# Optimization experiments

Measured on AMD Instinct MI355X. Metric: run time of the kernel, lower is better.

The kernel has to match this reference:

```python
import jax, jax.numpy as jnp
import numpy as np
import math

B, S, D = 16, 1, 4096
H, KVH, HD = 32, 8, 128
MAXB, MAXS = 16, 4096
R = H // KVH  # n_rep


def _rope(t, cos, sin):
    # t: [B, S, h, HD]; cos/sin: [S, HD//2]
    tf = t.astype(jnp.float32).reshape(*t.shape[:-1], HD // 2, 2)
    a, b = tf[..., 0], tf[..., 1]
    c = cos[None, :, None, :]
    s = sin[None, :, None, :]
    out = jnp.stack([a * c - b * s, a * s + b * c], axis=-1)
    return out.reshape(t.shape).astype(t.dtype)


def setup_inputs() -> dict:
    key = jax.random.key(0)
    ks = jax.random.split(key, 9)
    scale = 1.0 / math.sqrt(D)
    ang = jax.random.uniform(ks[7], (S, HD // 2), jnp.float32) * (2.0 * np.pi)
    return {
        "x": jax.random.normal(ks[0], (B, S, D), jnp.float32),
        "start_pos": 4095,
        "freqs_cos": jnp.cos(ang),
        "freqs_sin": jnp.sin(ang),
        "cache_k": jax.random.normal(ks[1], (MAXB, MAXS, KVH, HD), jnp.float32),
        "cache_v": jax.random.normal(ks[2], (MAXB, MAXS, KVH, HD), jnp.float32),
        "wq": jax.random.normal(ks[3], (D, H * HD), jnp.float32) * scale,
        "wk": jax.random.normal(ks[4], (D, KVH * HD), jnp.float32) * scale,
        "wv": jax.random.normal(ks[5], (D, KVH * HD), jnp.float32) * scale,
        "wo": jax.random.normal(ks[6], (H * HD, D), jnp.float32) * scale,
    }


def reference(x, start_pos, freqs_cos, freqs_sin, cache_k, cache_v, wq, wk, wv, wo):
    bsz, seqlen, _ = x.shape
    xq = (x @ wq).reshape(bsz, seqlen, H, HD)
    xk = (x @ wk).reshape(bsz, seqlen, KVH, HD)
    xv = (x @ wv).reshape(bsz, seqlen, KVH, HD)
    # rotary embeddings on q and k
    xq = _rope(xq, freqs_cos, freqs_sin)
    xk = _rope(xk, freqs_cos, freqs_sin)
    # KV-cache write (start_pos is a static Python int)
    cache_k = cache_k.at[:bsz, start_pos:start_pos + seqlen].set(xk)
    cache_v = cache_v.at[:bsz, start_pos:start_pos + seqlen].set(xv)
    T = start_pos + seqlen
    keys = cache_k[:bsz, :T]    # [B, T, KVH, HD]
    values = cache_v[:bsz, :T]  # [B, T, KVH, HD]
    # GQA: group q heads as [KVH, R] instead of materializing repeated K/V
    q = xq.reshape(bsz, seqlen, KVH, R, HD)
    scores = jnp.einsum("bsgrd,btgd->bgrst", q, keys) / math.sqrt(HD)
    probs = jax.nn.softmax(scores.astype(jnp.float32), axis=-1).astype(xq.dtype)
    out = jnp.einsum("bgrst,btgd->bsgrd", probs, values)
    out = out.reshape(bsz, seqlen, H * HD)
    return out @ wo
```

## Files before the change

kernel.cpp:

```cpp
#include <hip/hip_runtime.h>
#include <hip/hip_bf16.h>
#include <math.h>

#define B 16
#define D 4096
#define H 32
#define KVH 8
#define HD 128
#define R 4
#define T 4096
#define NQKV 6144
#define NCH_A 32
#define NCH_E 32
#define NCH64 64
#define MREC 516

#define OFF_QKV   0
#define SZ_QKV    (B*NQKV)
#define OFF_ATTN  (OFF_QKV + SZ_QKV)
#define SZ_ATTN   (B*H*HD)
#define OFF_MLO   (OFF_ATTN + SZ_ATTN)
#define SZ_MLO    (B*KVH*NCH64*MREC)
#define OFF_PART  (OFF_ATTN + SZ_ATTN)

__global__ __launch_bounds__(256) void gemv_qkv(
    const float* __restrict__ x, const float* __restrict__ wq,
    const float* __restrict__ wk, const float* __restrict__ wv,
    float* __restrict__ part) {
  int cb = blockIdx.x;
  int ch = blockIdx.y;
  int d0 = ch * 128;
  __shared__ float xT[128][20];
  for (int i = threadIdx.x; i < 128*B; i += 256) {
    int b = i >> 7;
    int d = i & 127;
    xT[d][b] = x[b*D + d0 + d];
  }
  __syncthreads();
  const float* W; int ncols, colbase, outbase;
  if (cb < 16)      { W = wq; ncols = 4096; colbase = cb*256;      outbase = colbase; }
  else if (cb < 20) { W = wk; ncols = 1024; colbase = (cb-16)*256; outbase = 4096 + colbase; }
  else              { W = wv; ncols = 1024; colbase = (cb-20)*256; outbase = 5120 + colbase; }
  int j = colbase + threadIdx.x;
  const float* wp = W + (size_t)d0*ncols + j;
  float acc[16];
  #pragma unroll
  for (int b = 0; b < 16; ++b) acc[b] = 0.f;
  for (int dd = 0; dd < 128; dd += 8) {
    float w[8];
    #pragma unroll
    for (int u = 0; u < 8; ++u) w[u] = wp[(size_t)u*ncols];
    wp += (size_t)8*ncols;
    #pragma unroll
    for (int u = 0; u < 8; ++u) {
      int d = dd + u;
      #pragma unroll
      for (int bq = 0; bq < 4; ++bq) {
        float4 xb = *(const float4*)&xT[d][bq*4];
        acc[bq*4+0] += w[u]*xb.x;
        acc[bq*4+1] += w[u]*xb.y;
        acc[bq*4+2] += w[u]*xb.z;
        acc[bq*4+3] += w[u]*xb.w;
      }
    }
  }
  int outcol = outbase + threadIdx.x;
  #pragma unroll
  for (int b = 0; b < 16; ++b) {
    part[(size_t)ch*SZ_QKV + b*NQKV + outcol] = acc[b];
  }
}

__global__ __launch_bounds__(256) void reduce_rope(
    const float* __restrict__ part, float* __restrict__ qkv,
    const float* __restrict__ fc, const float* __restrict__ fs) {
  int i = blockIdx.x*256 + threadIdx.x;
  int flat = i*2;
  float2 s = make_float2(0.f, 0.f);
  for (int c = 0; c < NCH_A; ++c) {
    float2 v = *(const float2*)&part[(size_t)c*SZ_QKV + flat];
    s.x += v.x; s.y += v.y;
  }
  int col = flat % NQKV;
  if (col < 5120) {
    int jj = (col & 127) >> 1;
    float c = fc[jj], sn = fs[jj];
    float ox = s.x*c - s.y*sn;
    float oy = s.x*sn + s.y*c;
    if (col < 4096) { ox *= 0.08838834764831845f; oy *= 0.08838834764831845f; }
    s.x = ox; s.y = oy;
  }
  *(float2*)&qkv[flat] = s;
}

__global__ __launch_bounds__(256) void attn_kernel(
    const float* __restrict__ qkv, const float* __restrict__ cache_k,
    const float* __restrict__ cache_v, float* __restrict__ mlo) {
  int chunk = blockIdx.x, gh = blockIdx.y, b = blockIdx.z;
  int tid = threadIdx.x, wave = tid >> 6, lane = tid & 63;
  int g = gh*4 + wave;
  int t0 = chunk * 64;
  __shared__ float4 q_lds4[4][4][32];
  __shared__ float4 p_lds[4][64];

  {
    const float* qp = qkv + b*NQKV + g*R*HD;
    int f = lane*2;
    q_lds4[wave][f>>5][f&31] = *(const float4*)(qp + f*4);
    f++;
    q_lds4[wave][f>>5][f&31] = *(const float4*)(qp + f*4);
  }

  const float* knew = qkv + b*NQKV + 4096 + g*HD;
  const float* vnew = qkv + b*NQKV + 5120 + g*HD;
  size_t base = ((size_t)(b*KVH + g)*NCH64 + chunk)*MREC;

  {
    int sub = lane & 7, rloc = lane >> 3;
    float l4[4] = {0.f,0.f,0.f,0.f};
    #pragma unroll 2
    for (int p = 0; p < 8; ++p) {
      int row = p*8 + rloc;
      int t = t0 + row;
      const float* kp = (t == T-1) ? knew
                        : &cache_k[(((size_t)b*T + t)*KVH + g)*HD];
      float4 kreg[4];
      #pragma unroll
      for (int i = 0; i < 4; ++i) kreg[i] = ((const float4*)kp)[i*8 + sub];
      float sA[4] = {0.f,0.f,0.f,0.f};
      #pragma unroll
      for (int i = 0; i < 4; ++i) {
        #pragma unroll
        for (int h = 0; h < 4; ++h) {
          float4 qv = q_lds4[wave][h][i*8 + sub];
          sA[h] += kreg[i].x*qv.x + kreg[i].y*qv.y + kreg[i].z*qv.z + kreg[i].w*qv.w;
        }
      }
      #pragma unroll
      for (int h = 0; h < 4; ++h) {
        sA[h] += __shfl_xor(sA[h], 1);
        sA[h] += __shfl_xor(sA[h], 2);
        sA[h] += __shfl_xor(sA[h], 4);
        sA[h] = __expf(sA[h]);
        l4[h] += sA[h];
      }
      if (sub == 0) p_lds[wave][row] = make_float4(sA[0], sA[1], sA[2], sA[3]);
    }
    #pragma unroll
    for (int h = 0; h < 4; ++h) {
      l4[h] += __shfl_xor(l4[h], 8);
      l4[h] += __shfl_xor(l4[h], 16);
      l4[h] += __shfl_xor(l4[h], 32);
    }
    if (lane == 0) {
      mlo[base + 0] = l4[0]; mlo[base + 1] = l4[1];
      mlo[base + 2] = l4[2]; mlo[base + 3] = l4[3];
    }
  }

  {
    int sub = lane & 31, rhalf = lane >> 5;
    float4 acc4[4];
    #pragma unroll
    for (int h = 0; h < 4; ++h) acc4[h] = make_float4(0.f,0.f,0.f,0.f);
    #pragma unroll 2
    for (int bt = 0; bt < 8; ++bt) {
      float4 vreg[4];
      #pragma unroll
      for (int i = 0; i < 4; ++i) {
        int row = bt*8 + i*2 + rhalf;
        int t = t0 + row;
        const float* vrow = (t == T-1) ? vnew
                           : &cache_v[(((size_t)b*T + t)*KVH + g)*HD];
        vreg[i] = *(const float4*)&vrow[sub*4];
      }
      #pragma unroll
      for (int i = 0; i < 4; ++i) {
        int row = bt*8 + i*2 + rhalf;
        float4 p = p_lds[wave][row];
        acc4[0].x += p.x*vreg[i].x; acc4[0].y += p.x*vreg[i].y;
        acc4[0].z += p.x*vreg[i].z; acc4[0].w += p.x*vreg[i].w;
        acc4[1].x += p.y*vreg[i].x; acc4[1].y += p.y*vreg[i].y;
        acc4[1].z += p.y*vreg[i].z; acc4[1].w += p.y*vreg[i].w;
        acc4[2].x += p.z*vreg[i].x; acc4[2].y += p.z*vreg[i].y;
        acc4[2].z += p.z*vreg[i].z; acc4[2].w += p.z*vreg[i].w;
        acc4[3].x += p.w*vreg[i].x; acc4[3].y += p.w*vreg[i].y;
        acc4[3].z += p.w*vreg[i].z; acc4[3].w += p.w*vreg[i].w;
      }
    }
    #pragma unroll
    for (int h = 0; h < 4; ++h) {
      acc4[h].x += __shfl_xor(acc4[h].x, 32);
      acc4[h].y += __shfl_xor(acc4[h].y, 32);
      acc4[h].z += __shfl_xor(acc4[h].z, 32);
      acc4[h].w += __shfl_xor(acc4[h].w, 32);
    }
    if (rhalf == 0) {
      #pragma unroll
      for (int h = 0; h < 4; ++h)
        *(float4*)&mlo[base + 4 + h*HD + sub*4] = acc4[h];
    }
  }
}

__global__ __launch_bounds__(128) void combine_kernel(
    const float* __restrict__ mlo, float* __restrict__ attn) {
  int g = blockIdx.x, b = blockIdx.y;
  int d = threadIdx.x;
  size_t b0 = (size_t)(b*KVH + g)*NCH64*MREC;
  #pragma unroll
  for (int h = 0; h < 4; ++h) {
    float l = 0.f, o = 0.f;
    for (int c = 0; c < NCH64; ++c) {
      size_t bb = b0 + (size_t)c*MREC;
      l += mlo[bb + h];
      o += mlo[bb + 4 + h*HD + d];
    }
    attn[b*D + (g*R + h)*HD + d] = o / l;
  }
}

__global__ __launch_bounds__(256) void gemv_out(
    const float* __restrict__ attn, const float* __restrict__ wo,
    float* __restrict__ part) {
  int cb = blockIdx.x;
  int ch = blockIdx.y;
  int d0 = ch * 128;
  __shared__ float xT[128][20];
  for (int i = threadIdx.x; i < 128*B; i += 256) {
    int b = i >> 7;
    int d = i & 127;
    xT[d][b] = attn[b*D + d0 + d];
  }
  __syncthreads();
  int j = cb*256 + threadIdx.x;
  const float* wp = wo + (size_t)d0*D + j;
  float acc[16];
  #pragma unroll
  for (int b = 0; b < 16; ++b) acc[b] = 0.f;
  for (int dd = 0; dd < 128; dd += 8) {
    float w[8];
    #pragma unroll
    for (int u = 0; u < 8; ++u) w[u] = wp[(size_t)u*D];
    wp += (size_t)8*D;
    #pragma unroll
    for (int u = 0; u < 8; ++u) {
      int d = dd + u;
      #pragma unroll
      for (int bq = 0; bq < 4; ++bq) {
        float4 xb = *(const float4*)&xT[d][bq*4];
        acc[bq*4+0] += w[u]*xb.x;
        acc[bq*4+1] += w[u]*xb.y;
        acc[bq*4+2] += w[u]*xb.z;
        acc[bq*4+3] += w[u]*xb.w;
      }
    }
  }
  #pragma unroll
  for (int b = 0; b < 16; ++b) {
    part[(size_t)ch*SZ_ATTN + b*D + j] = acc[b];
  }
}

__global__ __launch_bounds__(256) void reduce_part(
    const float* __restrict__ part, float* __restrict__ out, int n, int nch) {
  int i = (blockIdx.x*256 + threadIdx.x)*4;
  if (i >= n) return;
  float4 s = make_float4(0.f,0.f,0.f,0.f);
  for (int c = 0; c < nch; ++c) {
    float4 v = *(const float4*)&part[(size_t)c*n + i];
    s.x += v.x; s.y += v.y; s.z += v.z; s.w += v.w;
  }
  *(float4*)&out[i] = s;
}

extern "C" void kernel_launch(void* const* d_in, const int* in_sizes, int n_in,
                              void* d_out, int out_size, void* d_ws, size_t ws_size,
                              hipStream_t stream) {
  const float* x  = (const float*)d_in[0];
  const float* fc = (const float*)d_in[2];
  const float* fs = (const float*)d_in[3];
  const float* ck = (const float*)d_in[4];
  const float* cv = (const float*)d_in[5];
  const float* wq = (const float*)d_in[6];
  const float* wk = (const float*)d_in[7];
  const float* wv = (const float*)d_in[8];
  const float* wo = (const float*)d_in[9];
  float* out  = (float*)d_out;
  float* ws   = (float*)d_ws;
  float* qkv  = ws + OFF_QKV;
  float* attn = ws + OFF_ATTN;
  float* mlo  = ws + OFF_MLO;
  float* part = ws + OFF_PART;

  gemv_qkv<<<dim3(24, NCH_A), 256, 0, stream>>>(x, wq, wk, wv, part);
  reduce_rope<<<dim3(SZ_QKV/512), 256, 0, stream>>>(part, qkv, fc, fs);
  attn_kernel<<<dim3(NCH64, 2, B), 256, 0, stream>>>(qkv, ck, cv, mlo);
  combine_kernel<<<dim3(KVH, B), 128, 0, stream>>>(mlo, attn);
  gemv_out<<<dim3(16, NCH_E), 256, 0, stream>>>(attn, wo, part);
  reduce_part<<<dim3(SZ_ATTN/1024), 256, 0, stream>>>(part, out, SZ_ATTN, NCH_E);
}
```

Baseline: 183.8 us.

## Restructure decode attention: one block per batch chunk over all KV heads, with max-stabilized softmax

Each attention block now covers all 8 KV heads for a 64-token chunk of one batch, so every K/V row (1024 contiguous floats) is read fully coalesced. K is staged through LDS with a one-step register prefetch. Scores go to a shared score tile, and a per-chunk max-subtracted softmax replaces the unstabilized exp. The combine kernel now rescales each chunk by its max and runs one block per query head. The trade-offs are fewer, larger blocks (1024 instead of 2048), more LDS per block, extra syncthreads, and a larger partial-result record per chunk.

```diff
diff --git a/kernel.cpp b/kernel.cpp
--- a/kernel.cpp
+++ b/kernel.cpp
@@ -13,14 +13,14 @@
 #define NCH_A 32
 #define NCH_E 32
 #define NCH64 64
-#define MREC 516
+#define MREC 4160
 
 #define OFF_QKV   0
 #define SZ_QKV    (B*NQKV)
 #define OFF_ATTN  (OFF_QKV + SZ_QKV)
 #define SZ_ATTN   (B*H*HD)
 #define OFF_MLO   (OFF_ATTN + SZ_ATTN)
-#define SZ_MLO    (B*KVH*NCH64*MREC)
+#define SZ_MLO    (B*NCH64*MREC)
 #define OFF_PART  (OFF_ATTN + SZ_ATTN)
 
 __global__ __launch_bounds__(256) void gemv_qkv(
@@ -96,44 +96,56 @@
 __global__ __launch_bounds__(256) void attn_kernel(
     const float* __restrict__ qkv, const float* __restrict__ cache_k,
     const float* __restrict__ cache_v, float* __restrict__ mlo) {
-  int chunk = blockIdx.x, gh = blockIdx.y, b = blockIdx.z;
+  int chunk = blockIdx.x, b = blockIdx.y;
   int tid = threadIdx.x, wave = tid >> 6, lane = tid & 63;
-  int g = gh*4 + wave;
   int t0 = chunk * 64;
-  __shared__ float4 q_lds4[4][4][32];
-  __shared__ float4 p_lds[4][64];
+  int g0 = wave * 2;
+  __shared__ float4 ktile[4][4][2][35];
+  __shared__ float score[64][36];
+
+  size_t base = ((size_t)b*NCH64 + chunk)*MREC;
 
   {
-    const float* qp = qkv + b*NQKV + g*R*HD;
-    int f = lane*2;
-    q_lds4[wave][f>>5][f&31] = *(const float4*)(qp + f*4);
-    f++;
-    q_lds4[wave][f>>5][f&31] = *(const float4*)(qp + f*4);
-  }
-
-  const float* knew = qkv + b*NQKV + 4096 + g*HD;
-  const float* vnew = qkv + b*NQKV + 5120 + g*HD;
-  size_t base = ((size_t)(b*KVH + g)*NCH64 + chunk)*MREC;
-
-  {
-    int sub = lane & 7, rloc = lane >> 3;
-    float l4[4] = {0.f,0.f,0.f,0.f};
-    #pragma unroll 2
-    for (int p = 0; p < 8; ++p) {
-      int row = p*8 + rloc;
-      int t = t0 + row;
-      const float* kp = (t == T-1) ? knew
-                        : &cache_k[(((size_t)b*T + t)*KVH + g)*HD];
-      float4 kreg[4];
-      #pragma unroll
-      for (int i = 0; i < 4; ++i) kreg[i] = ((const float4*)kp)[i*8 + sub];
+    int sub = lane & 7, rowg = lane >> 3;
+    int krow = rowg >> 1, kgsel = rowg & 1;
+    int kg = g0 + kgsel;
+    float4 qreg[4][4];
+    #pragma unroll
+    for (int h = 0; h < 4; ++h)
+      #pragma unroll
+      for (int i = 0; i < 4; ++i)
+        qreg[h][i] = *(const float4*)(qkv + b*NQKV + (kg*4 + h)*HD + (i*8 + sub)*4);
+
+    const float* kbase = cache_k + (size_t)b*T*1024 + g0*HD;
+    const float* knew  = qkv + b*NQKV + 4096 + g0*HD;
+    float4 cur[4];
+    #pragma unroll
+    for (int ii = 0; ii < 4; ++ii) {
+      int t = t0 + ii;
+      const float* src = (t == T-1) ? knew : kbase + (size_t)t*1024;
+      cur[ii] = *(const float4*)(src + lane*4);
+    }
+    for (int bt = 0; bt < 16; ++bt) {
+      float4 nxt[4];
+      if (bt < 15) {
+        #pragma unroll
+        for (int ii = 0; ii < 4; ++ii) {
+          int t = t0 + (bt+1)*4 + ii;
+          const float* src = (t == T-1) ? knew : kbase + (size_t)t*1024;
+          nxt[ii] = *(const float4*)(src + lane*4);
+        }
+      }
+      #pragma unroll
+      for (int ii = 0; ii < 4; ++ii)
+        ktile[wave][ii][lane >> 5][lane & 31] = cur[ii];
       float sA[4] = {0.f,0.f,0.f,0.f};
       #pragma unroll
       for (int i = 0; i < 4; ++i) {
+        float4 kf = ktile[wave][krow][kgsel][i*8 + sub];
         #pragma unroll
         for (int h = 0; h < 4; ++h) {
-          float4 qv = q_lds4[wave][h][i*8 + sub];
-          sA[h] += kreg[i].x*qv.x + kreg[i].y*qv.y + kreg[i].z*qv.z + kreg[i].w*qv.w;
+          sA[h] += kf.x*qreg[h][i].x + kf.y*qreg[h][i].y
+                 + kf.z*qreg[h][i].z + kf.w*qreg[h][i].w;
         }
       }
       #pragma unroll
@@ -141,83 +153,85 @@
         sA[h] += __shfl_xor(sA[h], 1);
         sA[h] += __shfl_xor(sA[h], 2);
         sA[h] += __shfl_xor(sA[h], 4);
-        sA[h] = __expf(sA[h]);
-        l4[h] += sA[h];
-      }
-      if (sub == 0) p_lds[wave][row] = make_float4(sA[0], sA[1], sA[2], sA[3]);
-    }
-    #pragma unroll
-    for (int h = 0; h < 4; ++h) {
-      l4[h] += __shfl_xor(l4[h], 8);
-      l4[h] += __shfl_xor(l4[h], 16);
-      l4[h] += __shfl_xor(l4[h], 32);
-    }
-    if (lane == 0) {
-      mlo[base + 0] = l4[0]; mlo[base + 1] = l4[1];
-      mlo[base + 2] = l4[2]; mlo[base + 3] = l4[3];
-    }
-  }
+      }
+      if (sub == 0)
+        *(float4*)&score[bt*4 + krow][kg*4] = make_float4(sA[0], sA[1], sA[2], sA[3]);
+      #pragma unroll
+      for (int ii = 0; ii < 4; ++ii) cur[ii] = nxt[ii];
+    }
+  }
+  __syncthreads();
 
   {
-    int sub = lane & 31, rhalf = lane >> 5;
+    int h = tid >> 3, rg = tid & 7;
+    float vv[8]; float m = -1e30f;
+    #pragma unroll
+    for (int i = 0; i < 8; ++i) { vv[i] = score[rg + i*8][h]; m = fmaxf(m, vv[i]); }
+    m = fmaxf(m, __shfl_xor(m, 1));
+    m = fmaxf(m, __shfl_xor(m, 2));
+    m = fmaxf(m, __shfl_xor(m, 4));
+    float l = 0.f;
+    #pragma unroll
+    for (int i = 0; i < 8; ++i) { float p = __expf(vv[i] - m); score[rg + i*8][h] = p; l += p; }
+    l += __shfl_xor(l, 1); l += __shfl_xor(l, 2); l += __shfl_xor(l, 4);
+    if (rg == 0) { mlo[base + h] = m; mlo[base + 32 + h] = l; }
+  }
+  __syncthreads();
+
+  {
+    int pos = lane & 31, gsel = lane >> 5;
+    int vg = g0 + gsel;
+    const float* vbase = cache_v + (size_t)b*T*1024 + g0*HD;
+    const float* vnew  = qkv + b*NQKV + 5120 + g0*HD;
     float4 acc4[4];
     #pragma unroll
     for (int h = 0; h < 4; ++h) acc4[h] = make_float4(0.f,0.f,0.f,0.f);
-    #pragma unroll 2
-    for (int bt = 0; bt < 8; ++bt) {
+    for (int bt = 0; bt < 16; ++bt) {
       float4 vreg[4];
       #pragma unroll
-      for (int i = 0; i < 4; ++i) {
-        int row = bt*8 + i*2 + rhalf;
-        int t = t0 + row;
-        const float* vrow = (t == T-1) ? vnew
-                           : &cache_v[(((size_t)b*T + t)*KVH + g)*HD];
-        vreg[i] = *(const float4*)&vrow[sub*4];
-      }
-      #pragma unroll
-      for (int i = 0; i < 4; ++i) {
-        int row = bt*8 + i*2 + rhalf;
-        float4 p = p_lds[wave][row];
-        acc4[0].x += p.x*vreg[i].x; acc4[0].y += p.x*vreg[i].y;
-        acc4[0].z += p.x*vreg[i].z; acc4[0].w += p.x*vreg[i].w;
-        acc4[1].x += p.y*vreg[i].x; acc4[1].y += p.y*vreg[i].y;
-        acc4[1].z += p.y*vreg[i].z; acc4[1].w += p.y*vreg[i].w;
-        acc4[2].x += p.z*vreg[i].x; acc4[2].y += p.z*vreg[i].y;
-        acc4[2].z += p.z*vreg[i].z; acc4[2].w += p.z*vreg[i].w;
-        acc4[3].x += p.w*vreg[i].x; acc4[3].y += p.w*vreg[i].y;
-        acc4[3].z += p.w*vreg[i].z; acc4[3].w += p.w*vreg[i].w;
-      }
-    }
-    #pragma unroll
-    for (int h = 0; h < 4; ++h) {
-      acc4[h].x += __shfl_xor(acc4[h].x, 32);
-      acc4[h].y += __shfl_xor(acc4[h].y, 32);
-      acc4[h].z += __shfl_xor(acc4[h].z, 32);
-      acc4[h].w += __shfl_xor(acc4[h].w, 32);
-    }
-    if (rhalf == 0) {
-      #pragma unroll
-      for (int h = 0; h < 4; ++h)
-        *(float4*)&mlo[base + 4 + h*HD + sub*4] = acc4[h];
-    }
+      for (int ii = 0; ii < 4; ++ii) {
+        int t = t0 + bt*4 + ii;
+        const float* src = (t == T-1) ? vnew : vbase + (size_t)t*1024;
+        vreg[ii] = *(const float4*)(src + lane*4);
+      }
+      #pragma unroll
+      for (int ii = 0; ii < 4; ++ii) {
+        float4 p = *(const float4*)&score[bt*4 + ii][vg*4];
+        acc4[0].x += p.x*vreg[ii].x; acc4[0].y += p.x*vreg[ii].y;
+        acc4[0].z += p.x*vreg[ii].z; acc4[0].w += p.x*vreg[ii].w;
+        acc4[1].x += p.y*vreg[ii].x; acc4[1].y += p.y*vreg[ii].y;
+        acc4[1].z += p.y*vreg[ii].z; acc4[1].w += p.y*vreg[ii].w;
+        acc4[2].x += p.z*vreg[ii].x; acc4[2].y += p.z*vreg[ii].y;
+        acc4[2].z += p.z*vreg[ii].z; acc4[2].w += p.z*vreg[ii].w;
+        acc4[3].x += p.w*vreg[ii].x; acc4[3].y += p.w*vreg[ii].y;
+        acc4[3].z += p.w*vreg[ii].z; acc4[3].w += p.w*vreg[ii].w;
+      }
+    }
+    #pragma unroll
+    for (int h = 0; h < 4; ++h)
+      *(float4*)&mlo[base + 64 + (size_t)(vg*4 + h)*HD + pos*4] = acc4[h];
   }
 }
 
 __global__ __launch_bounds__(128) void combine_kernel(
     const float* __restrict__ mlo, float* __restrict__ attn) {
-  int g = blockIdx.x, b = blockIdx.y;
+  int hh = blockIdx.x;
+  int b = blockIdx.y;
   int d = threadIdx.x;
-  size_t b0 = (size_t)(b*KVH + g)*NCH64*MREC;
-  #pragma unroll
-  for (int h = 0; h < 4; ++h) {
-    float l = 0.f, o = 0.f;
-    for (int c = 0; c < NCH64; ++c) {
-      size_t bb = b0 + (size_t)c*MREC;
-      l += mlo[bb + h];
-      o += mlo[bb + 4 + h*HD + d];
-    }
-    attn[b*D + (g*R + h)*HD + d] = o / l;
-  }
+  size_t base0 = (size_t)b*NCH64*MREC;
+  float mg = -1e30f;
+  #pragma unroll 8
+  for (int c = 0; c < NCH64; ++c)
+    mg = fmaxf(mg, mlo[base0 + (size_t)c*MREC + hh]);
+  float lg = 0.f, o = 0.f;
+  #pragma unroll 4
+  for (int c = 0; c < NCH64; ++c) {
+    size_t bb = base0 + (size_t)c*MREC;
+    float f = __expf(mlo[bb + hh] - mg);
+    lg += f*mlo[bb + 32 + hh];
+    o  += f*mlo[bb + 64 + (size_t)hh*HD + d];
+  }
+  attn[b*D + hh*HD + d] = o / lg;
 }
 
 __global__ __launch_bounds__(256) void gemv_out(
@@ -295,8 +309,8 @@
 
   gemv_qkv<<<dim3(24, NCH_A), 256, 0, stream>>>(x, wq, wk, wv, part);
   reduce_rope<<<dim3(SZ_QKV/512), 256, 0, stream>>>(part, qkv, fc, fs);
-  attn_kernel<<<dim3(NCH64, 2, B), 256, 0, stream>>>(qkv, ck, cv, mlo);
-  combine_kernel<<<dim3(KVH, B), 128, 0, stream>>>(mlo, attn);
+  attn_kernel<<<dim3(NCH64, B), 256, 0, stream>>>(qkv, ck, cv, mlo);
+  combine_kernel<<<dim3(H, B), 128, 0, stream>>>(mlo, attn);
   gemv_out<<<dim3(16, NCH_E), 256, 0, stream>>>(attn, wo, part);
   reduce_part<<<dim3(SZ_ATTN/1024), 256, 0, stream>>>(part, out, SZ_ATTN, NCH_E);
 }
```

After: 240.3 us. 30.8% more time.
